# Performance work log

Measured on AMD Instinct MI355X. Metric: run time of the kernel, lower is better.

## Reference

```python
import jax, jax.numpy as jnp
import numpy as np

R = 2048      # reservoir_size
I = 32        # input_size
O = 32        # output_size
T = 8192      # number of timesteps
SPECTRAL_RADIUS = 0.9


def setup_inputs() -> dict:
    key = jax.random.key(0)
    k1, k2, k3, k4 = jax.random.split(key, 4)
    X = jax.random.normal(k1, (T, I), dtype=jnp.float32)
    # W_in ~ U(-1, 1) as in the torch module
    W_in = jax.random.uniform(k2, (R, I), dtype=jnp.float32, minval=-1.0, maxval=1.0)
    # W_res: random sign-flipped matrix rescaled to target spectral radius.
    # For an iid Gaussian matrix the spectral radius is ~sqrt(R)*std, so
    # scaling by SPECTRAL_RADIUS/sqrt(R) reproduces the rescaling step.
    W_res = jax.random.normal(k3, (R, R), dtype=jnp.float32) * (SPECTRAL_RADIUS / np.sqrt(R))
    W_res = W_res.astype(jnp.float32)
    # W_out: readout over concat([state, input]) -> [O, R + I]
    W_out = jax.random.normal(k4, (O, R + I), dtype=jnp.float32) * 0.02
    state0 = jnp.zeros((R,), dtype=jnp.float32)
    return {"X": X, "W_in": W_in, "W_res": W_res, "W_out": W_out, "state0": state0}


def reference(X, W_in, W_res, W_out, state0):
    """ESN.predict: sequential tanh reservoir recurrence + linear readout.

    state_{t+1} = tanh(W_in @ x_t + W_res @ state_t)
    pred_t      = W_out @ concat([state_{t+1}, x_t])
    Loop runs over the first T-1 inputs (matches `range(X.shape[0]-1)`),
    and since output_size == input_size the torch code returns the T-1
    predictions (initial zero column dropped).
    """
    def step(state, x):  # state: [R], x: [I]
        new_state = jnp.tanh(W_in @ x + W_res @ state)
        pred = W_out @ jnp.concatenate([new_state, x])  # [O]
        return new_state, pred

    _, preds = jax.lax.scan(step, state0, X[:-1])
    return preds  # [T-1, O]
```

## Files before the change

### kernel.cpp

```cpp
#include <hip/hip_runtime.h>
#include <hip/hip_fp16.h>
#include <math.h>


#define R_    2048
#define I_    32
#define O_    32
#define NSTEP 8191
#define G_    256
#define BLK   256
#define TB    4
#define CAPP  (1u << 24)

typedef unsigned int u32;
typedef unsigned long long u64;

__device__ __forceinline__ float tanh_fast(float u) {
    float e = __expf(2.f * u);
    return 1.f - __fdividef(2.f, e + 1.f);
}
__device__ __forceinline__ u32 pkh(float v, u32 tag) {
    return (tag << 16) | (u32)__half_as_ushort(__float2half(v));
}
__device__ __forceinline__ u64 ald(const u64* p) {
    return __hip_atomic_load(p, __ATOMIC_RELAXED, __HIP_MEMORY_SCOPE_AGENT);
}
__device__ __forceinline__ float h2f(u32 b) {
    return __half2float(__ushort_as_half((unsigned short)(b & 0xFFFFu)));
}


__global__ __launch_bounds__(256) void esn_readout(const u32* __restrict__ states,
                                                   const float* __restrict__ W_out,
                                                   const float* __restrict__ X,
                                                   float* __restrict__ out)
{
    __shared__ float s_arr[TB][R_];
    const int t0  = blockIdx.x * TB;
    const int tid = threadIdx.x;
    #pragma unroll
    for (int i = 0; i < TB; ++i) {
        const int t = t0 + i;
        if (t < NSTEP) {
            const u64* p64 = (const u64*)(states + (size_t)(t + 1) * R_);
            #pragma unroll
            for (int q = 0; q < 4; ++q) {
                u64 a = *(const u64*)(&p64[q * 256 + tid]);
                float2 f; f.x = h2f((u32)a); f.y = h2f((u32)(a >> 32));
                *reinterpret_cast<float2*>(&s_arr[i][q * 512 + 2 * tid]) = f;
            }
        }
    }
    __syncthreads();
    const int o = tid >> 3, c = tid & 7;
    const float* wrow = W_out + (size_t)o * (R_ + I_) + c * 256;
    float a0 = 0.f, a1 = 0.f, a2 = 0.f, a3 = 0.f;
    #pragma unroll 8
    for (int j = 0; j < 256; j += 4) {
        float4 wv = *reinterpret_cast<const float4*>(wrow + j);
        float4 s0 = *reinterpret_cast<const float4*>(&s_arr[0][c * 256 + j]);
        float4 s1 = *reinterpret_cast<const float4*>(&s_arr[1][c * 256 + j]);
        float4 s2 = *reinterpret_cast<const float4*>(&s_arr[2][c * 256 + j]);
        float4 s3 = *reinterpret_cast<const float4*>(&s_arr[3][c * 256 + j]);
        a0 = fmaf(wv.x, s0.x, a0); a0 = fmaf(wv.y, s0.y, a0);
        a0 = fmaf(wv.z, s0.z, a0); a0 = fmaf(wv.w, s0.w, a0);
        a1 = fmaf(wv.x, s1.x, a1); a1 = fmaf(wv.y, s1.y, a1);
        a1 = fmaf(wv.z, s1.z, a1); a1 = fmaf(wv.w, s1.w, a1);
        a2 = fmaf(wv.x, s2.x, a2); a2 = fmaf(wv.y, s2.y, a2);
        a2 = fmaf(wv.z, s2.z, a2); a2 = fmaf(wv.w, s2.w, a2);
        a3 = fmaf(wv.x, s3.x, a3); a3 = fmaf(wv.y, s3.y, a3);
        a3 = fmaf(wv.z, s3.z, a3); a3 = fmaf(wv.w, s3.w, a3);
    }
    if (c == 7) {
        const float* wx = W_out + (size_t)o * (R_ + I_) + R_;
        #pragma unroll
        for (int j = 0; j < 32; j += 4) {
            float4 wv = *reinterpret_cast<const float4*>(wx + j);
            float4 x0 = *reinterpret_cast<const float4*>(X + (size_t)(t0 + 0) * I_ + j);
            a0 = fmaf(wv.x, x0.x, a0); a0 = fmaf(wv.y, x0.y, a0);
            a0 = fmaf(wv.z, x0.z, a0); a0 = fmaf(wv.w, x0.w, a0);
            if (t0 + 1 < NSTEP) {
                float4 x1 = *reinterpret_cast<const float4*>(X + (size_t)(t0 + 1) * I_ + j);
                a1 = fmaf(wv.x, x1.x, a1); a1 = fmaf(wv.y, x1.y, a1);
                a1 = fmaf(wv.z, x1.z, a1); a1 = fmaf(wv.w, x1.w, a1);
            }
            if (t0 + 2 < NSTEP) {
                float4 x2 = *reinterpret_cast<const float4*>(X + (size_t)(t0 + 2) * I_ + j);
                a2 = fmaf(wv.x, x2.x, a2); a2 = fmaf(wv.y, x2.y, a2);
                a2 = fmaf(wv.z, x2.z, a2); a2 = fmaf(wv.w, x2.w, a2);
            }
            if (t0 + 3 < NSTEP) {
                float4 x3 = *reinterpret_cast<const float4*>(X + (size_t)(t0 + 3) * I_ + j);
                a3 = fmaf(wv.x, x3.x, a3); a3 = fmaf(wv.y, x3.y, a3);
                a3 = fmaf(wv.z, x3.z, a3); a3 = fmaf(wv.w, x3.w, a3);
            }
        }
    }
    a0 += __shfl_xor(a0, 1, 64); a0 += __shfl_xor(a0, 2, 64); a0 += __shfl_xor(a0, 4, 64);
    a1 += __shfl_xor(a1, 1, 64); a1 += __shfl_xor(a1, 2, 64); a1 += __shfl_xor(a1, 4, 64);
    a2 += __shfl_xor(a2, 1, 64); a2 += __shfl_xor(a2, 2, 64); a2 += __shfl_xor(a2, 4, 64);
    a3 += __shfl_xor(a3, 1, 64); a3 += __shfl_xor(a3, 2, 64); a3 += __shfl_xor(a3, 4, 64);
    if (c == 0) {
        out[(t0 + 0) * O_ + o] = a0;
        if (t0 + 1 < NSTEP) out[(t0 + 1) * O_ + o] = a1;
        if (t0 + 2 < NSTEP) out[(t0 + 2) * O_ + o] = a2;
        if (t0 + 3 < NSTEP) out[(t0 + 3) * O_ + o] = a3;
    }
}

__global__ __launch_bounds__(BLK)
__attribute__((amdgpu_waves_per_eu(1, 1)))
void esn_main(const float* __restrict__ X, const float* __restrict__ W_in,
              const float* __restrict__ W_res, const float* __restrict__ state0,
              u32* __restrict__ ring)
{
    const int tid = threadIdx.x;
    const int g   = blockIdx.x;
    __shared__ float s_lds[2][R_];

    const int lane  = tid & 63;
    const int wave  = tid >> 6;
    const int myrow = g * 8 + wave * 2;

    float w[2][32];
    #pragma unroll
    for (int i = 0; i < 2; ++i) {
        const float* wr = W_res + (size_t)(myrow + i) * R_;
        #pragma unroll
        for (int k = 0; k < 8; ++k) {
            float4 v = *reinterpret_cast<const float4*>(wr + k * 256 + 4 * lane);
            w[i][4*k+0] = v.x; w[i][4*k+1] = v.y;
            w[i][4*k+2] = v.z; w[i][4*k+3] = v.w;
        }
    }
    float wi[2];
    #pragma unroll
    for (int i = 0; i < 2; ++i)
        wi[i] = (lane < 32) ? W_in[(size_t)(myrow + i) * I_ + lane] : 0.f;

    #pragma unroll
    for (int q = 0; q < 8; ++q)
        s_lds[0][q * 256 + tid] = state0[q * 256 + tid];
    __syncthreads();

    float xl = (lane < 32) ? X[lane] : 0.f;

    for (int t = 0; t < NSTEP; ++t) {
        u64 b0 = 0, b1 = 0, b2 = 0, b3 = 0;
        const u64* p64 = (const u64*)(ring + (size_t)(t + 1) * R_);
        if (t < NSTEP - 1) {
            b0 = ald(&p64[0 * 256 + tid]);
            b1 = ald(&p64[1 * 256 + tid]);
            b2 = ald(&p64[2 * 256 + tid]);
            b3 = ald(&p64[3 * 256 + tid]);
        }

        const float* sbuf = s_lds[t & 1];
        float p0 = wi[0] * xl, p1 = wi[1] * xl;
        #pragma unroll
        for (int k = 0; k < 8; ++k) {
            const float4 sv = *reinterpret_cast<const float4*>(
                &sbuf[k * 256 + 4 * lane]);
            p0 = fmaf(w[0][4*k+0], sv.x, p0); p0 = fmaf(w[0][4*k+1], sv.y, p0);
            p0 = fmaf(w[0][4*k+2], sv.z, p0); p0 = fmaf(w[0][4*k+3], sv.w, p0);
            p1 = fmaf(w[1][4*k+0], sv.x, p1); p1 = fmaf(w[1][4*k+1], sv.y, p1);
            p1 = fmaf(w[1][4*k+2], sv.z, p1); p1 = fmaf(w[1][4*k+3], sv.w, p1);
        }

        float keep = (lane & 1) ? p1 : p0;
        float give = (lane & 1) ? p0 : p1;
        float A = keep + __shfl_xor(give, 1, 64);
        A += __shfl_xor(A, 2, 64);
        A += __shfl_xor(A, 4, 64);
        A += __shfl_xor(A, 8, 64);
        A += __shfl_xor(A, 16, 64);
        A += __shfl_xor(A, 32, 64);

        if (lane < 2) {
            __hip_atomic_store(&ring[(size_t)(t + 1) * R_ + myrow + lane],
                               pkh(tanh_fast(A), (u32)(t + 1)),
                               __ATOMIC_RELAXED, __HIP_MEMORY_SCOPE_AGENT);
        }
        if (t == NSTEP - 1) break;

        float xn = (lane < 32) ? X[(size_t)(t + 1) * I_ + lane] : 0.f;

        u64 a0 = 0, a1 = 0, a2 = 0, a3 = 0;
        {
            const u32 tg  = (u32)(t + 1);
            const u64 pat = ((u64)tg << 48) | ((u64)tg << 16);
            const u64 msk = 0xFFFF0000FFFF0000ull;
            unsigned pend = 0xFu;
            if (!((b0 ^ pat) & msk)) { a0 = b0; pend &= ~1u; }
            if (!((b1 ^ pat) & msk)) { a1 = b1; pend &= ~2u; }
            if (!((b2 ^ pat) & msk)) { a2 = b2; pend &= ~4u; }
            if (!((b3 ^ pat) & msk)) { a3 = b3; pend &= ~8u; }
            unsigned tries = 0;
            while (pend) {
                u64 c0 = 0, c1 = 0, c2 = 0, c3 = 0;
                if (pend & 1u) c0 = ald(&p64[0 * 256 + tid]);
                if (pend & 2u) c1 = ald(&p64[1 * 256 + tid]);
                if (pend & 4u) c2 = ald(&p64[2 * 256 + tid]);
                if (pend & 8u) c3 = ald(&p64[3 * 256 + tid]);
                if ((pend & 1u) && !((c0 ^ pat) & msk)) { a0 = c0; pend &= ~1u; }
                if ((pend & 2u) && !((c1 ^ pat) & msk)) { a1 = c1; pend &= ~2u; }
                if ((pend & 4u) && !((c2 ^ pat) & msk)) { a2 = c2; pend &= ~4u; }
                if ((pend & 8u) && !((c3 ^ pat) & msk)) { a3 = c3; pend &= ~8u; }
                if (!pend) break;
                if (++tries > CAPP) break;
                if (tries > 8) __builtin_amdgcn_s_sleep(1);
            }
        }
        {
            float* dbuf = s_lds[(t + 1) & 1];
            float2 f;
            f.x = h2f((u32)a0); f.y = h2f((u32)(a0 >> 32));
            *reinterpret_cast<float2*>(&dbuf[0 * 512 + 2 * tid]) = f;
            f.x = h2f((u32)a1); f.y = h2f((u32)(a1 >> 32));
            *reinterpret_cast<float2*>(&dbuf[1 * 512 + 2 * tid]) = f;
            f.x = h2f((u32)a2); f.y = h2f((u32)(a2 >> 32));
            *reinterpret_cast<float2*>(&dbuf[2 * 512 + 2 * tid]) = f;
            f.x = h2f((u32)a3); f.y = h2f((u32)(a3 >> 32));
            *reinterpret_cast<float2*>(&dbuf[3 * 512 + 2 * tid]) = f;
        }
        xl = xn;

        asm volatile("s_waitcnt lgkmcnt(0)" ::: "memory");
        __builtin_amdgcn_s_barrier();
        __builtin_amdgcn_sched_barrier(0);
    }
}

extern "C" void kernel_launch(void* const* d_in, const int* in_sizes, int n_in,
                              void* d_out, int out_size, void* d_ws, size_t ws_size,
                              hipStream_t stream)
{
    (void)in_sizes; (void)n_in; (void)out_size; (void)ws_size;
    const float* X      = (const float*)d_in[0];
    const float* W_in   = (const float*)d_in[1];
    const float* W_res  = (const float*)d_in[2];
    const float* W_out  = (const float*)d_in[3];
    const float* state0 = (const float*)d_in[4];
    float* out = (float*)d_out;

    u32* ring = (u32*)((char*)d_ws + 4096);

    hipLaunchKernelGGL(esn_main, dim3(G_), dim3(BLK), 0, stream,
                       X, W_in, W_res, state0, ring);
    hipLaunchKernelGGL(esn_readout, dim3((NSTEP + TB - 1) / TB), dim3(256), 0,
                       stream, ring, W_out, X, out);
}
```

Before: 8.862 ms.

## Use 512-thread blocks with one reservoir row per wave

Doubles the block to 8 waves so each wave computes a single reservoir row instead of two. Each thread now polls two 64-bit ring slots instead of four, which halves the per-thread work on the spin-wait and on the LDS state fill. It also drops the paired-row shuffle trick. The cost is more waves contending at the per-step barrier, and possibly different register pressure at 2 waves per EU.

```diff
diff --git a/kernel.cpp b/kernel.cpp
--- a/kernel.cpp
+++ b/kernel.cpp
@@ -8,7 +8,7 @@
 #define O_    32
 #define NSTEP 8191
 #define G_    256
-#define BLK   256
+#define BLK   512
 #define TB    4
 #define CAPP  (1u << 24)
 
@@ -109,7 +109,7 @@
 }
 
 __global__ __launch_bounds__(BLK)
-__attribute__((amdgpu_waves_per_eu(1, 1)))
+__attribute__((amdgpu_waves_per_eu(2, 2)))
 void esn_main(const float* __restrict__ X, const float* __restrict__ W_in,
               const float* __restrict__ W_res, const float* __restrict__ state0,
               u32* __restrict__ ring)
@@ -120,92 +120,75 @@
 
     const int lane  = tid & 63;
     const int wave  = tid >> 6;
-    const int myrow = g * 8 + wave * 2;
-
-    float w[2][32];
-    #pragma unroll
-    for (int i = 0; i < 2; ++i) {
-        const float* wr = W_res + (size_t)(myrow + i) * R_;
+    const int myrow = g * 8 + wave;
+
+    float w[32];
+    {
+        const float* wr = W_res + (size_t)myrow * R_;
         #pragma unroll
         for (int k = 0; k < 8; ++k) {
             float4 v = *reinterpret_cast<const float4*>(wr + k * 256 + 4 * lane);
-            w[i][4*k+0] = v.x; w[i][4*k+1] = v.y;
-            w[i][4*k+2] = v.z; w[i][4*k+3] = v.w;
-        }
-    }
-    float wi[2];
+            w[4*k+0] = v.x; w[4*k+1] = v.y; w[4*k+2] = v.z; w[4*k+3] = v.w;
+        }
+    }
+    const float wi = (lane < 32) ? W_in[(size_t)myrow * I_ + lane] : 0.f;
+
     #pragma unroll
-    for (int i = 0; i < 2; ++i)
-        wi[i] = (lane < 32) ? W_in[(size_t)(myrow + i) * I_ + lane] : 0.f;
-
-    #pragma unroll
-    for (int q = 0; q < 8; ++q)
-        s_lds[0][q * 256 + tid] = state0[q * 256 + tid];
+    for (int q = 0; q < 4; ++q)
+        s_lds[0][q * 512 + tid] = state0[q * 512 + tid];
     __syncthreads();
 
     float xl = (lane < 32) ? X[lane] : 0.f;
 
     for (int t = 0; t < NSTEP; ++t) {
-        u64 b0 = 0, b1 = 0, b2 = 0, b3 = 0;
+        u64 b0 = 0, b1 = 0;
         const u64* p64 = (const u64*)(ring + (size_t)(t + 1) * R_);
         if (t < NSTEP - 1) {
-            b0 = ald(&p64[0 * 256 + tid]);
-            b1 = ald(&p64[1 * 256 + tid]);
-            b2 = ald(&p64[2 * 256 + tid]);
-            b3 = ald(&p64[3 * 256 + tid]);
+            b0 = ald(&p64[tid]);
+            b1 = ald(&p64[512 + tid]);
         }
 
         const float* sbuf = s_lds[t & 1];
-        float p0 = wi[0] * xl, p1 = wi[1] * xl;
+        float p = wi * xl;
         #pragma unroll
         for (int k = 0; k < 8; ++k) {
             const float4 sv = *reinterpret_cast<const float4*>(
                 &sbuf[k * 256 + 4 * lane]);
-            p0 = fmaf(w[0][4*k+0], sv.x, p0); p0 = fmaf(w[0][4*k+1], sv.y, p0);
-            p0 = fmaf(w[0][4*k+2], sv.z, p0); p0 = fmaf(w[0][4*k+3], sv.w, p0);
-            p1 = fmaf(w[1][4*k+0], sv.x, p1); p1 = fmaf(w[1][4*k+1], sv.y, p1);
-            p1 = fmaf(w[1][4*k+2], sv.z, p1); p1 = fmaf(w[1][4*k+3], sv.w, p1);
-        }
-
-        float keep = (lane & 1) ? p1 : p0;
-        float give = (lane & 1) ? p0 : p1;
-        float A = keep + __shfl_xor(give, 1, 64);
-        A += __shfl_xor(A, 2, 64);
-        A += __shfl_xor(A, 4, 64);
-        A += __shfl_xor(A, 8, 64);
-        A += __shfl_xor(A, 16, 64);
-        A += __shfl_xor(A, 32, 64);
-
-        if (lane < 2) {
-            __hip_atomic_store(&ring[(size_t)(t + 1) * R_ + myrow + lane],
-                               pkh(tanh_fast(A), (u32)(t + 1)),
+            p = fmaf(w[4*k+0], sv.x, p); p = fmaf(w[4*k+1], sv.y, p);
+            p = fmaf(w[4*k+2], sv.z, p); p = fmaf(w[4*k+3], sv.w, p);
+        }
+
+        p += __shfl_xor(p, 1, 64);
+        p += __shfl_xor(p, 2, 64);
+        p += __shfl_xor(p, 4, 64);
+        p += __shfl_xor(p, 8, 64);
+        p += __shfl_xor(p, 16, 64);
+        p += __shfl_xor(p, 32, 64);
+
+        if (lane == 0) {
+            __hip_atomic_store(&ring[(size_t)(t + 1) * R_ + myrow],
+                               pkh(tanh_fast(p), (u32)(t + 1)),
                                __ATOMIC_RELAXED, __HIP_MEMORY_SCOPE_AGENT);
         }
         if (t == NSTEP - 1) break;
 
         float xn = (lane < 32) ? X[(size_t)(t + 1) * I_ + lane] : 0.f;
 
-        u64 a0 = 0, a1 = 0, a2 = 0, a3 = 0;
+        u64 a0 = 0, a1 = 0;
         {
             const u32 tg  = (u32)(t + 1);
             const u64 pat = ((u64)tg << 48) | ((u64)tg << 16);
             const u64 msk = 0xFFFF0000FFFF0000ull;
-            unsigned pend = 0xFu;
+            unsigned pend = 0x3u;
             if (!((b0 ^ pat) & msk)) { a0 = b0; pend &= ~1u; }
             if (!((b1 ^ pat) & msk)) { a1 = b1; pend &= ~2u; }
-            if (!((b2 ^ pat) & msk)) { a2 = b2; pend &= ~4u; }
-            if (!((b3 ^ pat) & msk)) { a3 = b3; pend &= ~8u; }
             unsigned tries = 0;
             while (pend) {
-                u64 c0 = 0, c1 = 0, c2 = 0, c3 = 0;
-                if (pend & 1u) c0 = ald(&p64[0 * 256 + tid]);
-                if (pend & 2u) c1 = ald(&p64[1 * 256 + tid]);
-                if (pend & 4u) c2 = ald(&p64[2 * 256 + tid]);
-                if (pend & 8u) c3 = ald(&p64[3 * 256 + tid]);
+                u64 c0 = 0, c1 = 0;
+                if (pend & 1u) c0 = ald(&p64[tid]);
+                if (pend & 2u) c1 = ald(&p64[512 + tid]);
                 if ((pend & 1u) && !((c0 ^ pat) & msk)) { a0 = c0; pend &= ~1u; }
                 if ((pend & 2u) && !((c1 ^ pat) & msk)) { a1 = c1; pend &= ~2u; }
-                if ((pend & 4u) && !((c2 ^ pat) & msk)) { a2 = c2; pend &= ~4u; }
-                if ((pend & 8u) && !((c3 ^ pat) & msk)) { a3 = c3; pend &= ~8u; }
                 if (!pend) break;
                 if (++tries > CAPP) break;
                 if (tries > 8) __builtin_amdgcn_s_sleep(1);
@@ -215,13 +198,9 @@
             float* dbuf = s_lds[(t + 1) & 1];
             float2 f;
             f.x = h2f((u32)a0); f.y = h2f((u32)(a0 >> 32));
-            *reinterpret_cast<float2*>(&dbuf[0 * 512 + 2 * tid]) = f;
+            *reinterpret_cast<float2*>(&dbuf[2 * tid]) = f;
             f.x = h2f((u32)a1); f.y = h2f((u32)(a1 >> 32));
-            *reinterpret_cast<float2*>(&dbuf[1 * 512 + 2 * tid]) = f;
-            f.x = h2f((u32)a2); f.y = h2f((u32)(a2 >> 32));
-            *reinterpret_cast<float2*>(&dbuf[2 * 512 + 2 * tid]) = f;
-            f.x = h2f((u32)a3); f.y = h2f((u32)(a3 >> 32));
-            *reinterpret_cast<float2*>(&dbuf[3 * 512 + 2 * tid]) = f;
+            *reinterpret_cast<float2*>(&dbuf[1024 + 2 * tid]) = f;
         }
         xl = xn;
 
```

Result: slower. 34.94 ms (+294.3%).
